# Optimization experiments

Hardware: AMD Instinct MI355X
Metric: run time of the kernel (lower is better)

## Reference

```python
import jax, jax.numpy as jnp
import numpy as np

N, E = 20000, 320000
IN_DIM, EDGE_DIM, HID = 64, 16, 64
# (in_c, heads, channels, out_c) per layer; last layer heads=1, concat=False
DIMS = [(64, 4, 64, 256), (256, 4, 64, 256), (256, 1, 64, 64)]


def _ln(x, g, b):
    m = x.mean(-1, keepdims=True)
    v = x.var(-1, keepdims=True)
    return (x - m) / jnp.sqrt(v + 1e-5) * g + b


def _gatv2(x, ei, ea, Wl, bl, Wr, br, We, att, bc, concat):
    # PyG GATv2Conv, eval mode (no dropout), add_self_loops=True, fill_value='mean'
    n = x.shape[0]
    H, C = att.shape
    ar = jnp.arange(n, dtype=ei.dtype)
    src = jnp.concatenate([ei[0], ar])
    dst = jnp.concatenate([ei[1], ar])
    ea_f = jnp.concatenate([ea, jnp.broadcast_to(ea.mean(0), (n, ea.shape[1]))], 0)
    xl = (x @ Wl + bl).reshape(n, H, C)   # source transform
    xr = (x @ Wr + br).reshape(n, H, C)   # target transform
    ee = (ea_f @ We).reshape(-1, H, C)    # edge transform (no bias in PyG)
    e = jax.nn.leaky_relu(xl[src] + xr[dst] + ee, 0.2)       # [E+N, H, C]
    score = jnp.einsum('ehc,hc->eh', e, att)                 # [E+N, H]
    mx = jax.ops.segment_max(score, dst, num_segments=n)
    a = jnp.exp(score - mx[dst])
    a = a / (jax.ops.segment_sum(a, dst, num_segments=n)[dst] + 1e-16)
    out = jax.ops.segment_sum(a[:, :, None] * xl[src], dst, num_segments=n)  # [N,H,C]
    out = out.reshape(n, H * C) if concat else out.mean(1)
    return out + bc


def _forward(x, eis, eas, Wp, bp, gp, bep, layers):
    h = jax.nn.gelu(_ln(x @ Wp + bp, gp, bep), approximate=False)
    for i in range(3):
        Wl, bl, Wr, br, We, att, bc, g, be, Wsk, bsk = layers[i]
        res = h @ Wsk + bsk
        h = _gatv2(h, eis[i], eas[i], Wl, bl, Wr, br, We, att, bc, i < 2)
        h = jax.nn.gelu(_ln(h, g, be), approximate=False) + res
    return h


def setup_inputs() -> dict:
    key = jax.random.key(0)
    ks = iter(jax.random.split(key, 64))
    rn = lambda shape, s=0.05: jax.random.normal(next(ks), shape, jnp.float32) * s
    d = {'x': jax.random.normal(next(ks), (N, IN_DIM), jnp.float32)}
    for i in range(3):
        d['ei%d' % i] = jax.random.randint(next(ks), (2, E), 0, N, jnp.int32)
        d['ea%d' % i] = jax.random.normal(next(ks), (E, EDGE_DIM), jnp.float32)
    d['Wp'] = rn((IN_DIM, HID)); d['bp'] = jnp.zeros(HID)
    d['gp'] = jnp.ones(HID); d['bep'] = jnp.zeros(HID)
    for i, (ic, H, C, oc) in enumerate(DIMS):
        hc = H * C
        d['Wl%d' % i] = rn((ic, hc)); d['bl%d' % i] = jnp.zeros(hc)
        d['Wr%d' % i] = rn((ic, hc)); d['br%d' % i] = jnp.zeros(hc)
        d['We%d' % i] = rn((EDGE_DIM, hc))
        d['att%d' % i] = rn((H, C), 0.1)
        d['bc%d' % i] = jnp.zeros(hc if i < 2 else C)
        d['g%d' % i] = jnp.ones(oc); d['be%d' % i] = jnp.zeros(oc)
        d['Wsk%d' % i] = rn((ic, oc)); d['bsk%d' % i] = jnp.zeros(oc)
    return d


def reference(x, ei0, ea0, ei1, ea1, ei2, ea2, Wp, bp, gp, bep,
              Wl0, bl0, Wr0, br0, We0, att0, bc0, g0, be0, Wsk0, bsk0,
              Wl1, bl1, Wr1, br1, We1, att1, bc1, g1, be1, Wsk1, bsk1,
              Wl2, bl2, Wr2, br2, We2, att2, bc2, g2, be2, Wsk2, bsk2):
    layers = [
        (Wl0, bl0, Wr0, br0, We0, att0, bc0, g0, be0, Wsk0, bsk0),
        (Wl1, bl1, Wr1, br1, We1, att1, bc1, g1, be1, Wsk1, bsk1),
        (Wl2, bl2, Wr2, br2, We2, att2, bc2, g2, be2, Wsk2, bsk2),
    ]
    return _forward(x, (ei0, ei1, ei2), (ea0, ea1, ea2), Wp, bp, gp, bep, layers)
```

## Files before the change

### kernel.cpp

```cpp
#include <hip/hip_runtime.h>
#include <hip/hip_bf16.h>
#include <math.h>

#define NV 20000
#define NE 320000
#define CSR_PAD 16

typedef __attribute__((ext_vector_type(8))) short bf16x8;
typedef __attribute__((ext_vector_type(4))) float f32x4;
typedef __attribute__((ext_vector_type(2))) _Float16 h2;

static __device__ __forceinline__ ushort f2b(float f) {
  __hip_bfloat16 h = __float2bfloat16(f);
  return *reinterpret_cast<ushort*>(&h);
}
static __device__ __forceinline__ float b2f(ushort u) {
  union { ushort s[2]; float f; } c;
  c.s[0] = 0; c.s[1] = u;
  return c.f;
}
static __device__ __forceinline__ ushort f2h(float f) {
  _Float16 h = (_Float16)f;
  return *reinterpret_cast<ushort*>(&h);
}
static __device__ __forceinline__ float blo(unsigned u) { return __uint_as_float(u << 16); }
static __device__ __forceinline__ float bhi(unsigned u) { return __uint_as_float(u & 0xffff0000u); }

static __device__ __forceinline__ float wave_sum64(float x) {
  x += __int_as_float(__builtin_amdgcn_update_dpp(0, __float_as_int(x), 0x111, 0xF, 0xF, true));
  x += __int_as_float(__builtin_amdgcn_update_dpp(0, __float_as_int(x), 0x112, 0xF, 0xF, true));
  x += __int_as_float(__builtin_amdgcn_update_dpp(0, __float_as_int(x), 0x114, 0xF, 0xF, true));
  x += __int_as_float(__builtin_amdgcn_update_dpp(0, __float_as_int(x), 0x118, 0xF, 0xF, true));
  x += __int_as_float(__builtin_amdgcn_update_dpp(0, __float_as_int(x), 0x142, 0xA, 0xF, true));
  x += __int_as_float(__builtin_amdgcn_update_dpp(0, __float_as_int(x), 0x143, 0xC, 0xF, true));
  return __int_as_float(__builtin_amdgcn_readlane(__float_as_int(x), 63));
}

static __device__ __forceinline__ float sum16(float x) {
  x += __int_as_float(__builtin_amdgcn_update_dpp(0, __float_as_int(x), 0x121, 0xF, 0xF, true));
  x += __int_as_float(__builtin_amdgcn_update_dpp(0, __float_as_int(x), 0x122, 0xF, 0xF, true));
  x += __int_as_float(__builtin_amdgcn_update_dpp(0, __float_as_int(x), 0x124, 0xF, 0xF, true));
  x += __int_as_float(__builtin_amdgcn_update_dpp(0, __float_as_int(x), 0x128, 0xF, 0xF, true));
  return x;
}

static __device__ __forceinline__ float dot16h(const uint4* __restrict__ E,
                                               const h2* __restrict__ Wch) {
#if __has_builtin(__builtin_amdgcn_fdot2)
  const h2* e = (const h2*)E;
  float s = 0.f;
#pragma unroll
  for (int j = 0; j < 8; ++j) s = __builtin_amdgcn_fdot2(e[j], Wch[j], s, false);
  return s;
#else
  const unsigned* u = (const unsigned*)E;
  float s = 0.f;
#pragma unroll
  for (int j = 0; j < 8; ++j) {
    union { unsigned v; h2 h; } cv; cv.v = u[j];
    s = fmaf((float)cv.h[0], (float)Wch[j][0], s);
    s = fmaf((float)cv.h[1], (float)Wch[j][1], s);
  }
  return s;
#endif
}

struct HArgs {
  const int* ei[3]; int* counts;
  const float* ea[3]; float* easum[3];
};

__global__ __launch_bounds__(256) void hist_kernel(HArgs a) {
  const int t = threadIdx.x, b = (int)blockIdx.x;
  if (b < 3750) {
    int gi = b * 256 + t;
    int l = gi / NE, i = gi - l * NE;
    atomicAdd(&a.counts[(size_t)l * (NV + 1) + a.ei[l][NE + i]], 1);
  } else {
    const int cb = b - 3750;
    const int l = cb >> 8, blk = cb & 255;
    const float4* ea4 = (const float4*)a.ea[l];
    const int cg = t & 3;
    int r = blk * 64 + (t >> 2);
    const int rstride = 256 * 64;
    float4 s = make_float4(0.f, 0.f, 0.f, 0.f);
    for (; r < NE; r += rstride) {
      float4 v = ea4[(size_t)r * 4 + cg];
      s.x += v.x; s.y += v.y; s.z += v.z; s.w += v.w;
    }
    __shared__ float4 red4[256];
    red4[t] = s;
    __syncthreads();
    if (t < 4) {
      float4 tot = make_float4(0.f, 0.f, 0.f, 0.f);
      for (int j = t; j < 256; j += 4) {
        float4 v = red4[j];
        tot.x += v.x; tot.y += v.y; tot.z += v.z; tot.w += v.w;
      }
      atomicAdd(&a.easum[l][t * 4 + 0], tot.x);
      atomicAdd(&a.easum[l][t * 4 + 1], tot.y);
      atomicAdd(&a.easum[l][t * 4 + 2], tot.z);
      atomicAdd(&a.easum[l][t * 4 + 3], tot.w);
    }
  }
}

struct CJob { const float* src; ushort* dst; int K, M; };
struct K2Args {
  const int* counts; int* offs; int* cursor;
  CJob jobs[9];
  unsigned* csr[3]; ushort* eab[3];
  const float *x, *Wp, *bp, *gp, *bep;
  ushort* h0;
};

__global__ __launch_bounds__(1024) void scan_proj_kernel(K2Args a) {
  const int b = blockIdx.x, t = threadIdx.x;
  if (b < 3) {
    const int* counts = a.counts + b * (NV + 1);
    int* offs = a.offs + b * (NV + 1);
    int* cursor = a.cursor + b * NV;
    __shared__ int ws[16];
    __shared__ int wexcl[17];
    const int lane = t & 63, wid = t >> 6;
    const int base = t * 20;
    int v[20];
    int tot = 0;
#pragma unroll
    for (int j = 0; j < 20; ++j) {
      int i = base + j;
      v[j] = (i < NV) ? counts[i] : 0;
      tot += v[j];
    }
    int x = tot;
#pragma unroll
    for (int o = 1; o < 64; o <<= 1) {
      int yy = __shfl_up(x, o, 64);
      if (lane >= o) x += yy;
    }
    if (lane == 63) ws[wid] = x;
    __syncthreads();
    if (t == 0) {
      int r = 0;
#pragma unroll
      for (int j = 0; j < 16; ++j) { wexcl[j] = r; r += ws[j]; }
      wexcl[16] = r;
    }
    __syncthreads();
    int run = wexcl[wid] + (x - tot);
#pragma unroll
    for (int j = 0; j < 20; ++j) {
      int i = base + j;
      if (i < NV) { offs[i] = run; cursor[i] = run; }
      run += v[j];
    }
    if (t == 0) offs[NV] = wexcl[16];
  } else if (b < 19) {
    if (b == 3 && t < 3 * CSR_PAD) {
      int l = t >> 4, p = t & 15;
      a.csr[l][NE + p] = 0u;
      uint4 z = make_uint4(0, 0, 0, 0);
      *(uint4*)(a.eab[l] + (size_t)(NE + p) * 16) = z;
      *(uint4*)(a.eab[l] + (size_t)(NE + p) * 16 + 8) = z;
    }
#pragma unroll
    for (int j = 0; j < 9; ++j) {
      CJob jb = a.jobs[j];
      const int total = jb.M * jb.K;
      for (int i = (b - 3) * 1024 + t; i < total; i += 16 * 1024) {
        int m = i / jb.K, k = i - m * jb.K;
        jb.dst[i] = f2b(jb.src[(size_t)k * jb.M + m]);
      }
    }
  } else {
    const int wid = t >> 6, lane = t & 63;
    const int row = (b - 19) * 16 + wid;
    float xv = a.x[(size_t)row * 64 + lane];
    float acc = a.bp[lane];
#pragma unroll
    for (int k = 0; k < 64; ++k) {
      float v = __shfl(xv, k, 64);
      acc = fmaf(v, a.Wp[k * 64 + lane], acc);
    }
    float s1 = wave_sum64(acc), s2 = wave_sum64(acc * acc);
    float mean = s1 * (1.0f / 64.0f);
    float var  = s2 * (1.0f / 64.0f) - mean * mean;
    float yv = (acc - mean) * rsqrtf(var + 1e-5f) * a.gp[lane] + a.bep[lane];
    float gel = 0.5f * yv * (1.0f + erff(yv * 0.70710678118654752f));
    a.h0[(size_t)row * 64 + lane] = f2b(gel);
  }
}

struct K3Args {
  const ushort *A, *WT;
  const float *b0, *b1, *b2;
  ushort *O0, *O1; float* O2;
  int K, M1, M2, Mtot, NT;
  const int* ei[3]; const float* ea[3];
  int* cursor;
  unsigned* csr[3]; ushort* eab[3]; int HC[3];
};

__global__ __launch_bounds__(256) void mega_kernel(K3Args a) {
  __shared__ ushort As[128][40];
  __shared__ ushort Bs[64][40];
  const int t = threadIdx.x;
  const int b = (int)blockIdx.x;
  if (b < a.NT) {
    const int wave = t >> 6, lane = t & 63;
    const int mcols = a.Mtot >> 6;
    const int col0 = (b % mcols) * 64, row0 = (b / mcols) * 128;
    const int m_ = lane & 15, q = lane >> 4;
    f32x4 acc[2][4];
#pragma unroll
    for (int i = 0; i < 2; ++i)
#pragma unroll
      for (int j = 0; j < 4; ++j) acc[i][j] = (f32x4){0.f, 0.f, 0.f, 0.f};
    const int ar = t >> 1, ac = (t & 1) * 16;
    const int br = t >> 2, bcol = (t & 3) * 8;
    const ushort* Ap = a.A + (size_t)(row0 + ar) * a.K + ac;
    const ushort* Bp = a.WT + (size_t)(col0 + br) * a.K + bcol;
    const bool a_ok = (row0 + ar) < NV;
    for (int k0 = 0; k0 < a.K; k0 += 32) {
      uint4 av0 = make_uint4(0, 0, 0, 0), av1 = make_uint4(0, 0, 0, 0);
      if (a_ok) { av0 = *(const uint4*)(Ap + k0); av1 = *(const uint4*)(Ap + k0 + 8); }
      uint4 bv = *(const uint4*)(Bp + k0);
      *(uint4*)&As[ar][ac] = av0;
      *(uint4*)&As[ar][ac + 8] = av1;
      *(uint4*)&Bs[br][bcol] = bv;
      __syncthreads();
      bf16x8 a0 = *(const bf16x8*)&As[wave * 32 + m_][q * 8];
      bf16x8 a1 = *(const bf16x8*)&As[wave * 32 + 16 + m_][q * 8];
#pragma unroll
      for (int cf = 0; cf < 4; ++cf) {
        bf16x8 bfr = *(const bf16x8*)&Bs[cf * 16 + m_][q * 8];
        acc[0][cf] = __builtin_amdgcn_mfma_f32_16x16x32_bf16(a0, bfr, acc[0][cf], 0, 0, 0);
        acc[1][cf] = __builtin_amdgcn_mfma_f32_16x16x32_bf16(a1, bfr, acc[1][cf], 0, 0, 0);
      }
      __syncthreads();
    }
    const float* bias; int base, mode, Wd;
    if (col0 < a.M1)      { bias = a.b0; base = 0;    mode = 0; Wd = a.M1; }
    else if (col0 < a.M2) { bias = a.b1; base = a.M1; mode = 1; Wd = a.M2 - a.M1; }
    else                  { bias = a.b2; base = a.M2; mode = 2; Wd = a.Mtot - a.M2; }
#pragma unroll
    for (int rf = 0; rf < 2; ++rf) {
#pragma unroll
      for (int cf = 0; cf < 4; ++cf) {
        int col = col0 + cf * 16 + m_ - base;
        float bb = bias[col];
#pragma unroll
        for (int r = 0; r < 4; ++r) {
          int row = row0 + wave * 32 + rf * 16 + q * 4 + r;
          if (row < NV) {
            float v = acc[rf][cf][r] + bb;
            if (mode == 0)      a.O0[(size_t)row * Wd + col] = f2b(v);
            else if (mode == 1) a.O1[(size_t)row * Wd + col] = f2b(v);
            else                a.O2[(size_t)row * Wd + col] = v;
          }
        }
      }
    }
  } else {
    int gi = (b - a.NT) * 256 + t;
    int l = gi / NE, i = gi - l * NE;
    int dst = a.ei[l][NE + i], src = a.ei[l][i];
    int pos = atomicAdd(&a.cursor[(size_t)l * NV + dst], 1);
    a.csr[l][pos] = (unsigned)(src * a.HC[l]);
    const float4* er = (const float4*)(a.ea[l] + (size_t)i * 16);
    float4 q0 = er[0], q1 = er[1], q2 = er[2], q3 = er[3];
    uint4 w0, w1;
    w0.x = (unsigned)f2h(q0.x) | ((unsigned)f2h(q0.y) << 16);
    w0.y = (unsigned)f2h(q0.z) | ((unsigned)f2h(q0.w) << 16);
    w0.z = (unsigned)f2h(q1.x) | ((unsigned)f2h(q1.y) << 16);
    w0.w = (unsigned)f2h(q1.z) | ((unsigned)f2h(q1.w) << 16);
    w1.x = (unsigned)f2h(q2.x) | ((unsigned)f2h(q2.y) << 16);
    w1.y = (unsigned)f2h(q2.z) | ((unsigned)f2h(q2.w) << 16);
    w1.z = (unsigned)f2h(q3.x) | ((unsigned)f2h(q3.y) << 16);
    w1.w = (unsigned)f2h(q3.z) | ((unsigned)f2h(q3.w) << 16);
    *(uint4*)(a.eab[l] + (size_t)pos * 16) = w0;
    *(uint4*)(a.eab[l] + (size_t)pos * 16 + 8) = w1;
  }
}

__global__ __launch_bounds__(256) void gemm_fused(
    const ushort* __restrict__ A, const ushort* __restrict__ WT,
    const float* __restrict__ b0, const float* __restrict__ b1,
    const float* __restrict__ b2,
    ushort* __restrict__ O0, ushort* __restrict__ O1, float* __restrict__ O2,
    int N, int K, int M1, int M2, int Mtot)
{
  __shared__ ushort As[128][40];
  __shared__ ushort Bs[64][40];
  const int t = threadIdx.x, wave = t >> 6, lane = t & 63;
  const int row0 = blockIdx.y * 128, col0 = blockIdx.x * 64;
  const int m_ = lane & 15, q = lane >> 4;
  f32x4 acc[2][4];
#pragma unroll
  for (int i = 0; i < 2; ++i)
#pragma unroll
    for (int j = 0; j < 4; ++j) acc[i][j] = (f32x4){0.f, 0.f, 0.f, 0.f};
  const int ar = t >> 1, ac = (t & 1) * 16;
  const int br = t >> 2, bcol = (t & 3) * 8;
  const ushort* Ap = A + (size_t)(row0 + ar) * K + ac;
  const ushort* Bp = WT + (size_t)(col0 + br) * K + bcol;
  const bool a_ok = (row0 + ar) < N;
  for (int k0 = 0; k0 < K; k0 += 32) {
    uint4 av0 = make_uint4(0, 0, 0, 0), av1 = make_uint4(0, 0, 0, 0);
    if (a_ok) { av0 = *(const uint4*)(Ap + k0); av1 = *(const uint4*)(Ap + k0 + 8); }
    uint4 bv = *(const uint4*)(Bp + k0);
    *(uint4*)&As[ar][ac] = av0;
    *(uint4*)&As[ar][ac + 8] = av1;
    *(uint4*)&Bs[br][bcol] = bv;
    __syncthreads();
    bf16x8 a0 = *(const bf16x8*)&As[wave * 32 + m_][q * 8];
    bf16x8 a1 = *(const bf16x8*)&As[wave * 32 + 16 + m_][q * 8];
#pragma unroll
    for (int cf = 0; cf < 4; ++cf) {
      bf16x8 bfr = *(const bf16x8*)&Bs[cf * 16 + m_][q * 8];
      acc[0][cf] = __builtin_amdgcn_mfma_f32_16x16x32_bf16(a0, bfr, acc[0][cf], 0, 0, 0);
      acc[1][cf] = __builtin_amdgcn_mfma_f32_16x16x32_bf16(a1, bfr, acc[1][cf], 0, 0, 0);
    }
    __syncthreads();
  }
  const float* bias; int base, mode, Wd;
  if (col0 < M1)      { bias = b0; base = 0;  mode = 0; Wd = M1; }
  else if (col0 < M2) { bias = b1; base = M1; mode = 1; Wd = M2 - M1; }
  else                { bias = b2; base = M2; mode = 2; Wd = Mtot - M2; }
#pragma unroll
  for (int rf = 0; rf < 2; ++rf) {
#pragma unroll
    for (int cf = 0; cf < 4; ++cf) {
      int col = col0 + cf * 16 + m_ - base;
      float bb = bias[col];
#pragma unroll
      for (int r = 0; r < 4; ++r) {
        int row = row0 + wave * 32 + rf * 16 + q * 4 + r;
        if (row < N) {
          float v = acc[rf][cf][r] + bb;
          if (mode == 0)      O0[(size_t)row * Wd + col] = f2b(v);
          else if (mode == 1) O1[(size_t)row * Wd + col] = f2b(v);
          else                O2[(size_t)row * Wd + col] = v;
        }
      }
    }
  }
}

__global__ __launch_bounds__(256) void agg4_kernel(
    const ushort* __restrict__ eab, const float* __restrict__ easum,
    const float* __restrict__ We,
    const ushort* __restrict__ xl, const ushort* __restrict__ xr,
    const float* __restrict__ att, const float* __restrict__ bc,
    const float* __restrict__ g, const float* __restrict__ be,
    const float* __restrict__ res,
    const int* __restrict__ offs, const unsigned* __restrict__ csr,
    ushort* __restrict__ houtb, int E)
{
  const int t = threadIdx.x, lane = t & 63, wave = t >> 6;
  const int n = blockIdx.x * 4 + wave;
  const int cb = 4 * lane;
  const size_t rowb = (size_t)n * 256 + cb;
  const float L2E = 1.4426950408889634f;

  float4 atv = *(const float4*)(att + cb);
  float at[4] = {atv.x * L2E, atv.y * L2E, atv.z * L2E, atv.w * L2E};

  h2 Wch[4][8];
  float esf[4] = {0.f, 0.f, 0.f, 0.f};
#pragma unroll
  for (int k = 0; k < 8; ++k) {
    float4 wr0 = *(const float4*)(We + (2 * k) * 256 + cb);
    float4 wr1 = *(const float4*)(We + (2 * k + 1) * 256 + cb);
    const float* w0 = &wr0.x;
    const float* w1 = &wr1.x;
    float e0 = easum[2 * k], e1 = easum[2 * k + 1];
#pragma unroll
    for (int j = 0; j < 4; ++j) {
      esf[j] = fmaf(e0, w0[j], esf[j]);
      esf[j] = fmaf(e1, w1[j], esf[j]);
      Wch[j][k] = (h2){(_Float16)w0[j], (_Float16)w1[j]};
    }
  }
#pragma unroll
  for (int j = 0; j < 4; ++j) esf[j] *= 1.0f / (float)E;

  uint2 qr = *(const uint2*)(xr + rowb);
  float xrv[4] = {blo(qr.x), bhi(qr.x), blo(qr.y), bhi(qr.y)};
  uint2 qn = *(const uint2*)(xl + rowb);
  float xln[4] = {blo(qn.x), bhi(qn.x), blo(qn.y), bhi(qn.y)};

  float p = 0.f;
#pragma unroll
  for (int j = 0; j < 4; ++j) {
    float v = xln[j] + xrv[j] + esf[j];
    v = v > 0.f ? v : 0.2f * v;
    p = fmaf(v, at[j], p);
  }
  float wself = exp2f(sum16(p));
  float acc[4];
#pragma unroll
  for (int j = 0; j < 4; ++j) acc[j] = wself * xln[j];
  float denom = wself;

  const int beg = __builtin_amdgcn_readfirstlane(offs[n]);
  const int end = __builtin_amdgcn_readfirstlane(offs[n + 1]);

  unsigned P[2];
  uint4 EA[2][2];
  uint2 XL[2];
#pragma unroll
  for (int k = 0; k < 2; ++k) {
    P[k] = csr[beg + k];
    const uint4* ep = (const uint4*)(eab + (size_t)(beg + k) * 16);
    EA[k][0] = ep[0]; EA[k][1] = ep[1];
  }
#pragma unroll
  for (int k = 0; k < 2; ++k)
    XL[k] = *(const uint2*)(xl + __builtin_amdgcn_readfirstlane(P[k]) + cb);

  for (int idx = beg; idx < end; idx += 2) {
    unsigned Q[2];
    uint4 EB[2][2];
    uint2 XN[2];
#pragma unroll
    for (int k = 0; k < 2; ++k) Q[k] = csr[idx + 2 + k];
#pragma unroll
    for (int k = 0; k < 2; ++k) {
      const uint4* ep = (const uint4*)(eab + (size_t)(idx + 2 + k) * 16);
      EB[k][0] = ep[0]; EB[k][1] = ep[1];
    }
#pragma unroll
    for (int k = 0; k < 2; ++k)
      XN[k] = *(const uint2*)(xl + __builtin_amdgcn_readfirstlane(Q[k]) + cb);

#pragma unroll
    for (int k = 0; k < 2; ++k) {
      float xf[4] = {blo(XL[k].x), bhi(XL[k].x), blo(XL[k].y), bhi(XL[k].y)};
      float pp = 0.f;
#pragma unroll
      for (int j = 0; j < 4; ++j) {
        float ee = dot16h(EA[k], Wch[j]);
        float v = xf[j] + xrv[j] + ee;
        v = v > 0.f ? v : 0.2f * v;
        pp = fmaf(v, at[j], pp);
      }
      float S = sum16(pp);
      float w = (idx + k < end) ? exp2f(S) : 0.f;
#pragma unroll
      for (int j = 0; j < 4; ++j) acc[j] = fmaf(w, xf[j], acc[j]);
      denom += w;
    }
#pragma unroll
    for (int k = 0; k < 2; ++k) { P[k] = Q[k]; EA[k][0] = EB[k][0]; EA[k][1] = EB[k][1]; XL[k] = XN[k]; }
  }

  const float inv = 1.0f / (denom + 1e-16f);
  float4 bcv = *(const float4*)(bc + cb);
  float out[4];
  out[0] = acc[0] * inv + bcv.x; out[1] = acc[1] * inv + bcv.y;
  out[2] = acc[2] * inv + bcv.z; out[3] = acc[3] * inv + bcv.w;

  float so1 = out[0] + out[1] + out[2] + out[3];
  float so2 = out[0] * out[0] + out[1] * out[1] + out[2] * out[2] + out[3] * out[3];
  float s1 = wave_sum64(so1), s2 = wave_sum64(so2);
  float mean = s1 * (1.0f / 256.0f);
  float var  = s2 * (1.0f / 256.0f) - mean * mean;
  float rstd = rsqrtf(var + 1e-5f);
  float4 gv = *(const float4*)(g + cb);
  float4 bev = *(const float4*)(be + cb);
  float4 rv = *(const float4*)(res + rowb);
  const float* gp = &gv.x; const float* bep = &bev.x; const float* rp = &rv.x;
  ushort ob[4];
#pragma unroll
  for (int j = 0; j < 4; ++j) {
    float y = (out[j] - mean) * rstd * gp[j] + bep[j];
    float gel = 0.5f * y * (1.0f + erff(y * 0.70710678118654752f));
    ob[j] = f2b(gel + rp[j]);
  }
  uint2 ov;
  ov.x = (unsigned)ob[0] | ((unsigned)ob[1] << 16);
  ov.y = (unsigned)ob[2] | ((unsigned)ob[3] << 16);
  *(uint2*)(houtb + rowb) = ov;
}

__global__ __launch_bounds__(256, 4) void agg1_kernel(
    const ushort* __restrict__ eab, const float* __restrict__ easum,
    const float* __restrict__ We,
    const ushort* __restrict__ xl, const ushort* __restrict__ xr,
    const float* __restrict__ att, const float* __restrict__ bc,
    const float* __restrict__ g, const float* __restrict__ be,
    const float* __restrict__ res,
    const int* __restrict__ offs, const unsigned* __restrict__ csr,
    float* __restrict__ houtf, int E)
{
  const int HC = 64;
  const int t = threadIdx.x, lane = t & 63, wave = t >> 6;
  const int n = blockIdx.x * 4 + wave;
  const int c = lane;

  const float xr_t = b2f(xr[(size_t)n * HC + c]);
  const float att_t = att[c] * 1.4426950408889634f;
  float eself = 0.f;
  h2 Wch[8];
#pragma unroll
  for (int j = 0; j < 8; ++j) {
    float w0 = We[(2 * j) * HC + c], w1 = We[(2 * j + 1) * HC + c];
    eself = fmaf(easum[2 * j], w0, eself);
    eself = fmaf(easum[2 * j + 1], w1, eself);
    Wch[j] = (h2){(_Float16)w0, (_Float16)w1};
  }
  eself *= 1.0f / (float)E;

  const float xln = b2f(xl[(size_t)n * HC + c]);
  float vs = xln + xr_t + eself;
  vs = vs > 0.f ? vs : 0.2f * vs;
  const float wself = exp2f(wave_sum64(vs * att_t));
  float acc = wself * xln, denom = wself;

  const int beg = __builtin_amdgcn_readfirstlane(offs[n]);
  const int end = __builtin_amdgcn_readfirstlane(offs[n + 1]);

  unsigned P[4];
  uint4 EA[4][2];
  float XL[4];
#pragma unroll
  for (int k = 0; k < 4; ++k) {
    P[k] = csr[beg + k];
    const uint4* ep = (const uint4*)(eab + (size_t)(beg + k) * 16);
    EA[k][0] = ep[0]; EA[k][1] = ep[1];
  }
#pragma unroll
  for (int k = 0; k < 4; ++k)
    XL[k] = b2f(xl[__builtin_amdgcn_readfirstlane(P[k]) + c]);

  for (int idx = beg; idx < end; idx += 4) {
    unsigned Q[4];
    uint4 EB[4][2];
    float XLN[4];
#pragma unroll
    for (int k = 0; k < 4; ++k) Q[k] = csr[idx + 4 + k];
#pragma unroll
    for (int k = 0; k < 4; ++k) {
      const uint4* ep = (const uint4*)(eab + (size_t)(idx + 4 + k) * 16);
      EB[k][0] = ep[0]; EB[k][1] = ep[1];
    }
#pragma unroll
    for (int k = 0; k < 4; ++k)
      XLN[k] = b2f(xl[__builtin_amdgcn_readfirstlane(Q[k]) + c]);

    float wv[4];
#pragma unroll
    for (int k = 0; k < 4; ++k) {
      float ee = dot16h(EA[k], Wch);
      float v = XL[k] + xr_t + ee;
      v = v > 0.f ? v : 0.2f * v;
      float S = wave_sum64(v * att_t);
      wv[k] = (idx + k < end) ? exp2f(S) : 0.f;
    }
#pragma unroll
    for (int k = 0; k < 4; ++k) { acc = fmaf(wv[k], XL[k], acc); denom += wv[k]; }
#pragma unroll
    for (int k = 0; k < 4; ++k) {
      P[k] = Q[k]; EA[k][0] = EB[k][0]; EA[k][1] = EB[k][1]; XL[k] = XLN[k];
    }
  }

  float out = acc / (denom + 1e-16f) + bc[c];
  float s1 = wave_sum64(out), s2 = wave_sum64(out * out);
  float mean = s1 / (float)HC;
  float var  = s2 / (float)HC - mean * mean;
  float y = (out - mean) * rsqrtf(var + 1e-5f) * g[c] + be[c];
  float gel = 0.5f * y * (1.0f + erff(y * 0.70710678118654752f));
  houtf[(size_t)n * HC + c] = gel + res[(size_t)n * HC + c];
}

extern "C" void kernel_launch(void* const* d_in, const int* in_sizes, int n_in,
                              void* d_out, int out_size, void* d_ws, size_t ws_size,
                              hipStream_t stream)
{
  auto in = [&](int i) { return (const float*)d_in[i]; };

  const int ic[3] = {64, 256, 256}, hc[3] = {256, 256, 64}, oc[3] = {256, 256, 64};
  const int CSRN = NE + CSR_PAD;

  char* w = (char*)d_ws;
  size_t off = 0;
  auto alloc = [&](size_t bytes) { void* p = w + off; off = (off + bytes + 511) & ~(size_t)511; return p; };
  ushort* B1   = (ushort*)alloc((size_t)NV * 256 * 2);
  ushort* B2   = (ushort*)alloc((size_t)NV * 256 * 2);
  float*  B3   = (float*)alloc((size_t)NV * 256 * 4);
  ushort* h0bf = (ushort*)alloc((size_t)NV * 64 * 2);
  ushort* h1bf = (ushort*)alloc((size_t)NV * 256 * 2);
  ushort* h2bf = (ushort*)alloc((size_t)NV * 256 * 2);
  ushort* Wcat[3];
  for (int i = 0; i < 3; ++i)
    Wcat[i] = (ushort*)alloc((size_t)(2 * hc[i] + oc[i]) * ic[i] * 2);
  float*    easumA  = (float*)alloc(3 * 64);
  int*      countsA = (int*)alloc((size_t)3 * (NV + 1) * 4);
  int*      offsA   = (int*)alloc((size_t)3 * (NV + 1) * 4);
  int*      cursorA = (int*)alloc((size_t)3 * NV * 4);
  unsigned* csrA    = (unsigned*)alloc((size_t)3 * CSRN * 4);
  ushort*   eabA    = (ushort*)alloc((size_t)3 * CSRN * 16 * 2);

  hipMemsetAsync(easumA, 0, 512 + (size_t)3 * (NV + 1) * 4, stream);

  HArgs ha;
  for (int i = 0; i < 3; ++i) {
    ha.ei[i] = (const int*)d_in[1 + 2 * i];
    ha.ea[i] = in(2 + 2 * i);
    ha.easum[i] = easumA + i * 16;
  }
  ha.counts = countsA;
  hist_kernel<<<3750 + 768, 256, 0, stream>>>(ha);

  K2Args k2;
  k2.counts = countsA; k2.offs = offsA; k2.cursor = cursorA;
  for (int i = 0; i < 3; ++i) {
    k2.jobs[i * 3 + 0] = {in(11 + 11 * i), Wcat[i],                             ic[i], hc[i]};
    k2.jobs[i * 3 + 1] = {in(13 + 11 * i), Wcat[i] + (size_t)hc[i] * ic[i],     ic[i], hc[i]};
    k2.jobs[i * 3 + 2] = {in(20 + 11 * i), Wcat[i] + (size_t)2 * hc[i] * ic[i], ic[i], oc[i]};
    k2.csr[i] = csrA + (size_t)i * CSRN;
    k2.eab[i] = eabA + (size_t)i * CSRN * 16;
  }
  k2.x = in(0); k2.Wp = in(7); k2.bp = in(8); k2.gp = in(9); k2.bep = in(10);
  k2.h0 = h0bf;
  scan_proj_kernel<<<19 + NV / 16, 1024, 0, stream>>>(k2);

  K3Args ga;
  ga.A = h0bf; ga.WT = Wcat[0];
  ga.b0 = in(12); ga.b1 = in(14); ga.b2 = in(21);
  ga.O0 = B1; ga.O1 = B2; ga.O2 = B3;
  ga.K = 64; ga.M1 = 256; ga.M2 = 512; ga.Mtot = 768;
  ga.NT = (768 / 64) * ((NV + 127) / 128);
  for (int i = 0; i < 3; ++i) {
    ga.ei[i] = (const int*)d_in[1 + 2 * i];
    ga.ea[i] = in(2 + 2 * i);
    ga.csr[i] = csrA + (size_t)i * CSRN;
    ga.eab[i] = eabA + (size_t)i * CSRN * 16;
    ga.HC[i] = hc[i];
  }
  ga.cursor = cursorA;
  mega_kernel<<<ga.NT + 3750, 256, 0, stream>>>(ga);

  agg4_kernel<<<NV / 4, 256, 0, stream>>>(
      eabA + 0, easumA + 0, in(15), B1, B2, in(16), in(17), in(18), in(19),
      B3, offsA, csrA, h1bf, NE);

  gemm_fused<<<dim3(768 / 64, (NV + 127) / 128), 256, 0, stream>>>(
      h1bf, Wcat[1], in(23), in(25), in(32), B1, B2, B3, NV, 256, 256, 512, 768);

  agg4_kernel<<<NV / 4, 256, 0, stream>>>(
      eabA + (size_t)CSRN * 16, easumA + 16, in(26), B1, B2, in(27), in(28),
      in(29), in(30), B3, offsA + (NV + 1), csrA + (size_t)CSRN, h2bf, NE);

  gemm_fused<<<dim3(192 / 64, (NV + 127) / 128), 256, 0, stream>>>(
      h2bf, Wcat[2], in(34), in(36), in(43), B1, B2, B3, NV, 256, 64, 128, 192);

  agg1_kernel<<<NV / 4, 256, 0, stream>>>(
      eabA + (size_t)2 * CSRN * 16, easumA + 32, in(37), B1, B2, in(38), in(39),
      in(40), in(41), B3, offsA + 2 * (NV + 1), csrA + (size_t)2 * CSRN,
      (float*)d_out, NE);
}
```

Baseline: 542.1 us.

## Split each node's edge aggregation across two waves and precompute packed edge weights

The aggregation kernels now give each destination node two waves that walk even and odd CSR edges, then merge partial sums and denominators through shared memory, doubling the grid. The fp16-packed edge weights and the self-loop mean-edge term are precomputed once in an extra block of the scan kernel, so no wave repeats that setup. The edge dot product now seeds its accumulator with xl+xr to save an add. This targets per-node latency on long serial edge loops, at the cost of a block-wide sync, shared-memory traffic, and half the waves idling through the epilogue.

```diff
diff --git a/kernel.cpp b/kernel.cpp
--- a/kernel.cpp
+++ b/kernel.cpp
@@ -25,6 +25,9 @@
 }
 static __device__ __forceinline__ float blo(unsigned u) { return __uint_as_float(u << 16); }
 static __device__ __forceinline__ float bhi(unsigned u) { return __uint_as_float(u & 0xffff0000u); }
+static __device__ __forceinline__ h2 u2h2(unsigned u) {
+  union { unsigned v; h2 h; } c; c.v = u; return c.h;
+}
 
 static __device__ __forceinline__ float wave_sum64(float x) {
   x += __int_as_float(__builtin_amdgcn_update_dpp(0, __float_as_int(x), 0x111, 0xF, 0xF, true));
@@ -44,17 +47,16 @@
   return x;
 }
 
-static __device__ __forceinline__ float dot16h(const uint4* __restrict__ E,
-                                               const h2* __restrict__ Wch) {
+static __device__ __forceinline__ float dot16h_i(const uint4* __restrict__ E,
+                                                 const h2* __restrict__ Wch,
+                                                 float s) {
 #if __has_builtin(__builtin_amdgcn_fdot2)
   const h2* e = (const h2*)E;
-  float s = 0.f;
 #pragma unroll
   for (int j = 0; j < 8; ++j) s = __builtin_amdgcn_fdot2(e[j], Wch[j], s, false);
   return s;
 #else
   const unsigned* u = (const unsigned*)E;
-  float s = 0.f;
 #pragma unroll
   for (int j = 0; j < 8; ++j) {
     union { unsigned v; h2 h; } cv; cv.v = u[j];
@@ -112,6 +114,10 @@
   unsigned* csr[3]; ushort* eab[3];
   const float *x, *Wp, *bp, *gp, *bep;
   ushort* h0;
+  const float* easum;
+  const float* We[3];
+  unsigned* wchx[3];
+  float* esfO[3];
 };
 
 __global__ __launch_bounds__(1024) void scan_proj_kernel(K2Args a) {
@@ -172,7 +178,7 @@
         jb.dst[i] = f2b(jb.src[(size_t)k * jb.M + m]);
       }
     }
-  } else {
+  } else if (b < 19 + NV / 16) {
     const int wid = t >> 6, lane = t & 63;
     const int row = (b - 19) * 16 + wid;
     float xv = a.x[(size_t)row * 64 + lane];
@@ -188,6 +194,34 @@
     float yv = (acc - mean) * rsqrtf(var + 1e-5f) * a.gp[lane] + a.bep[lane];
     float gel = 0.5f * yv * (1.0f + erff(yv * 0.70710678118654752f));
     a.h0[(size_t)row * 64 + lane] = f2b(gel);
+  } else {
+    for (int i = t; i < 4608; i += 1024) {
+      int l, e;
+      if (i < 2048)      { l = 0; e = i; }
+      else if (i < 4096) { l = 1; e = i - 2048; }
+      else               { l = 2; e = i - 4096; }
+      const int hcl = (l == 2) ? 64 : 256;
+      int k8 = e / hcl, c = e - k8 * hcl;
+      const float* We = a.We[l];
+      a.wchx[l][e] = (unsigned)f2h(We[(2 * k8) * hcl + c]) |
+                     ((unsigned)f2h(We[(2 * k8 + 1) * hcl + c]) << 16);
+    }
+    for (int i = t; i < 576; i += 1024) {
+      int l, c;
+      if (i < 256)      { l = 0; c = i; }
+      else if (i < 512) { l = 1; c = i - 256; }
+      else              { l = 2; c = i - 512; }
+      const int hcl = (l == 2) ? 64 : 256;
+      const float* We = a.We[l];
+      const float* es = a.easum + l * 16;
+      float s = 0.f;
+#pragma unroll
+      for (int k8 = 0; k8 < 8; ++k8) {
+        s = fmaf(es[2 * k8], We[(2 * k8) * hcl + c], s);
+        s = fmaf(es[2 * k8 + 1], We[(2 * k8 + 1) * hcl + c], s);
+      }
+      a.esfO[l][c] = s * (1.0f / (float)NE);
+    }
   }
 }
 
@@ -348,17 +382,19 @@
 }
 
 __global__ __launch_bounds__(256) void agg4_kernel(
-    const ushort* __restrict__ eab, const float* __restrict__ easum,
-    const float* __restrict__ We,
+    const ushort* __restrict__ eab, const unsigned* __restrict__ wchx,
+    const float* __restrict__ esf,
     const ushort* __restrict__ xl, const ushort* __restrict__ xr,
     const float* __restrict__ att, const float* __restrict__ bc,
     const float* __restrict__ g, const float* __restrict__ be,
     const float* __restrict__ res,
     const int* __restrict__ offs, const unsigned* __restrict__ csr,
-    ushort* __restrict__ houtb, int E)
+    ushort* __restrict__ houtb)
 {
-  const int t = threadIdx.x, lane = t & 63, wave = t >> 6;
-  const int n = blockIdx.x * 4 + wave;
+  __shared__ float mrg[4][64][5];
+  const int t = threadIdx.x, lane = t & 63, wid = t >> 6;
+  const int n = blockIdx.x * 2 + (wid >> 1);
+  const int par = wid & 1;
   const int cb = 4 * lane;
   const size_t rowb = (size_t)n * 256 + cb;
   const float L2E = 1.4426950408889634f;
@@ -367,43 +403,37 @@
   float at[4] = {atv.x * L2E, atv.y * L2E, atv.z * L2E, atv.w * L2E};
 
   h2 Wch[4][8];
-  float esf[4] = {0.f, 0.f, 0.f, 0.f};
-#pragma unroll
-  for (int k = 0; k < 8; ++k) {
-    float4 wr0 = *(const float4*)(We + (2 * k) * 256 + cb);
-    float4 wr1 = *(const float4*)(We + (2 * k + 1) * 256 + cb);
-    const float* w0 = &wr0.x;
-    const float* w1 = &wr1.x;
-    float e0 = easum[2 * k], e1 = easum[2 * k + 1];
-#pragma unroll
-    for (int j = 0; j < 4; ++j) {
-      esf[j] = fmaf(e0, w0[j], esf[j]);
-      esf[j] = fmaf(e1, w1[j], esf[j]);
-      Wch[j][k] = (h2){(_Float16)w0[j], (_Float16)w1[j]};
-    }
-  }
-#pragma unroll
-  for (int j = 0; j < 4; ++j) esf[j] *= 1.0f / (float)E;
+#pragma unroll
+  for (int k8 = 0; k8 < 8; ++k8) {
+    uint4 wv = *(const uint4*)(wchx + k8 * 256 + cb);
+    Wch[0][k8] = u2h2(wv.x); Wch[1][k8] = u2h2(wv.y);
+    Wch[2][k8] = u2h2(wv.z); Wch[3][k8] = u2h2(wv.w);
+  }
+  float4 esfv = *(const float4*)(esf + cb);
+  const float* esfp = &esfv.x;
 
   uint2 qr = *(const uint2*)(xr + rowb);
   float xrv[4] = {blo(qr.x), bhi(qr.x), blo(qr.y), bhi(qr.y)};
   uint2 qn = *(const uint2*)(xl + rowb);
   float xln[4] = {blo(qn.x), bhi(qn.x), blo(qn.y), bhi(qn.y)};
 
-  float p = 0.f;
-#pragma unroll
-  for (int j = 0; j < 4; ++j) {
-    float v = xln[j] + xrv[j] + esf[j];
-    v = v > 0.f ? v : 0.2f * v;
-    p = fmaf(v, at[j], p);
-  }
-  float wself = exp2f(sum16(p));
-  float acc[4];
-#pragma unroll
-  for (int j = 0; j < 4; ++j) acc[j] = wself * xln[j];
-  float denom = wself;
-
-  const int beg = __builtin_amdgcn_readfirstlane(offs[n]);
+  float acc[4] = {0.f, 0.f, 0.f, 0.f};
+  float denom = 0.f;
+  if (par == 0) {
+    float p = 0.f;
+#pragma unroll
+    for (int j = 0; j < 4; ++j) {
+      float v = xln[j] + xrv[j] + esfp[j];
+      v = v > 0.f ? v : 0.2f * v;
+      p = fmaf(v, at[j], p);
+    }
+    float wself = exp2f(sum16(p));
+#pragma unroll
+    for (int j = 0; j < 4; ++j) acc[j] = wself * xln[j];
+    denom = wself;
+  }
+
+  const int beg = __builtin_amdgcn_readfirstlane(offs[n]) + par;
   const int end = __builtin_amdgcn_readfirstlane(offs[n + 1]);
 
   unsigned P[2];
@@ -411,23 +441,23 @@
   uint2 XL[2];
 #pragma unroll
   for (int k = 0; k < 2; ++k) {
-    P[k] = csr[beg + k];
-    const uint4* ep = (const uint4*)(eab + (size_t)(beg + k) * 16);
+    P[k] = csr[beg + 2 * k];
+    const uint4* ep = (const uint4*)(eab + (size_t)(beg + 2 * k) * 16);
     EA[k][0] = ep[0]; EA[k][1] = ep[1];
   }
 #pragma unroll
   for (int k = 0; k < 2; ++k)
     XL[k] = *(const uint2*)(xl + __builtin_amdgcn_readfirstlane(P[k]) + cb);
 
-  for (int idx = beg; idx < end; idx += 2) {
+  for (int idx = beg; idx < end; idx += 4) {
     unsigned Q[2];
     uint4 EB[2][2];
     uint2 XN[2];
 #pragma unroll
-    for (int k = 0; k < 2; ++k) Q[k] = csr[idx + 2 + k];
+    for (int k = 0; k < 2; ++k) Q[k] = csr[idx + 4 + 2 * k];
 #pragma unroll
     for (int k = 0; k < 2; ++k) {
-      const uint4* ep = (const uint4*)(eab + (size_t)(idx + 2 + k) * 16);
+      const uint4* ep = (const uint4*)(eab + (size_t)(idx + 4 + 2 * k) * 16);
       EB[k][0] = ep[0]; EB[k][1] = ep[1];
     }
 #pragma unroll
@@ -440,20 +470,31 @@
       float pp = 0.f;
 #pragma unroll
       for (int j = 0; j < 4; ++j) {
-        float ee = dot16h(EA[k], Wch[j]);
-        float v = xf[j] + xrv[j] + ee;
+        float v = dot16h_i(EA[k], Wch[j], xf[j] + xrv[j]);
         v = v > 0.f ? v : 0.2f * v;
         pp = fmaf(v, at[j], pp);
       }
       float S = sum16(pp);
-      float w = (idx + k < end) ? exp2f(S) : 0.f;
+      float w = (idx + 2 * k < end) ? exp2f(S) : 0.f;
 #pragma unroll
       for (int j = 0; j < 4; ++j) acc[j] = fmaf(w, xf[j], acc[j]);
       denom += w;
     }
 #pragma unroll
-    for (int k = 0; k < 2; ++k) { P[k] = Q[k]; EA[k][0] = EB[k][0]; EA[k][1] = EB[k][1]; XL[k] = XN[k]; }
-  }
+    for (int k = 0; k < 2; ++k) {
+      P[k] = Q[k]; EA[k][0] = EB[k][0]; EA[k][1] = EB[k][1]; XL[k] = XN[k];
+    }
+  }
+
+#pragma unroll
+  for (int j = 0; j < 4; ++j) mrg[wid][lane][j] = acc[j];
+  mrg[wid][lane][4] = denom;
+  __syncthreads();
+  const int pw = wid ^ 1;
+#pragma unroll
+  for (int j = 0; j < 4; ++j) acc[j] += mrg[pw][lane][j];
+  denom += mrg[pw][lane][4];
+  if (par) return;
 
   const float inv = 1.0f / (denom + 1e-16f);
   float4 bcv = *(const float4*)(bc + cb);
@@ -485,86 +526,88 @@
 }
 
 __global__ __launch_bounds__(256, 4) void agg1_kernel(
-    const ushort* __restrict__ eab, const float* __restrict__ easum,
-    const float* __restrict__ We,
+    const ushort* __restrict__ eab, const unsigned* __restrict__ wchx,
+    const float* __restrict__ esf,
     const ushort* __restrict__ xl, const ushort* __restrict__ xr,
     const float* __restrict__ att, const float* __restrict__ bc,
     const float* __restrict__ g, const float* __restrict__ be,
     const float* __restrict__ res,
     const int* __restrict__ offs, const unsigned* __restrict__ csr,
-    float* __restrict__ houtf, int E)
+    float* __restrict__ houtf)
 {
   const int HC = 64;
-  const int t = threadIdx.x, lane = t & 63, wave = t >> 6;
-  const int n = blockIdx.x * 4 + wave;
+  __shared__ float mrg[4][64][2];
+  const int t = threadIdx.x, lane = t & 63, wid = t >> 6;
+  const int n = blockIdx.x * 2 + (wid >> 1);
+  const int par = wid & 1;
   const int c = lane;
 
   const float xr_t = b2f(xr[(size_t)n * HC + c]);
   const float att_t = att[c] * 1.4426950408889634f;
-  float eself = 0.f;
   h2 Wch[8];
 #pragma unroll
-  for (int j = 0; j < 8; ++j) {
-    float w0 = We[(2 * j) * HC + c], w1 = We[(2 * j + 1) * HC + c];
-    eself = fmaf(easum[2 * j], w0, eself);
-    eself = fmaf(easum[2 * j + 1], w1, eself);
-    Wch[j] = (h2){(_Float16)w0, (_Float16)w1};
-  }
-  eself *= 1.0f / (float)E;
-
+  for (int k8 = 0; k8 < 8; ++k8) Wch[k8] = u2h2(wchx[k8 * 64 + c]);
+  const float eself = esf[c];
   const float xln = b2f(xl[(size_t)n * HC + c]);
-  float vs = xln + xr_t + eself;
-  vs = vs > 0.f ? vs : 0.2f * vs;
-  const float wself = exp2f(wave_sum64(vs * att_t));
-  float acc = wself * xln, denom = wself;
-
-  const int beg = __builtin_amdgcn_readfirstlane(offs[n]);
+
+  float acc = 0.f, denom = 0.f;
+  if (par == 0) {
+    float vs = xln + xr_t + eself;
+    vs = vs > 0.f ? vs : 0.2f * vs;
+    float wself = exp2f(wave_sum64(vs * att_t));
+    acc = wself * xln; denom = wself;
+  }
+
+  const int beg = __builtin_amdgcn_readfirstlane(offs[n]) + par;
   const int end = __builtin_amdgcn_readfirstlane(offs[n + 1]);
 
-  unsigned P[4];
-  uint4 EA[4][2];
-  float XL[4];
-#pragma unroll
-  for (int k = 0; k < 4; ++k) {
-    P[k] = csr[beg + k];
-    const uint4* ep = (const uint4*)(eab + (size_t)(beg + k) * 16);
+  unsigned P[2];
+  uint4 EA[2][2];
+  float XL[2];
+#pragma unroll
+  for (int k = 0; k < 2; ++k) {
+    P[k] = csr[beg + 2 * k];
+    const uint4* ep = (const uint4*)(eab + (size_t)(beg + 2 * k) * 16);
     EA[k][0] = ep[0]; EA[k][1] = ep[1];
   }
 #pragma unroll
-  for (int k = 0; k < 4; ++k)
+  for (int k = 0; k < 2; ++k)
     XL[k] = b2f(xl[__builtin_amdgcn_readfirstlane(P[k]) + c]);
 
   for (int idx = beg; idx < end; idx += 4) {
-    unsigned Q[4];
-    uint4 EB[4][2];
-    float XLN[4];
-#pragma unroll
-    for (int k = 0; k < 4; ++k) Q[k] = csr[idx + 4 + k];
-#pragma unroll
-    for (int k = 0; k < 4; ++k) {
-      const uint4* ep = (const uint4*)(eab + (size_t)(idx + 4 + k) * 16);
+    unsigned Q[2];
+    uint4 EB[2][2];
+    float XLN[2];
+#pragma unroll
+    for (int k = 0; k < 2; ++k) Q[k] = csr[idx + 4 + 2 * k];
+#pragma unroll
+    for (int k = 0; k < 2; ++k) {
+      const uint4* ep = (const uint4*)(eab + (size_t)(idx + 4 + 2 * k) * 16);
       EB[k][0] = ep[0]; EB[k][1] = ep[1];
     }
 #pragma unroll
-    for (int k = 0; k < 4; ++k)
+    for (int k = 0; k < 2; ++k)
       XLN[k] = b2f(xl[__builtin_amdgcn_readfirstlane(Q[k]) + c]);
 
-    float wv[4];
-#pragma unroll
-    for (int k = 0; k < 4; ++k) {
-      float ee = dot16h(EA[k], Wch);
-      float v = XL[k] + xr_t + ee;
+#pragma unroll
+    for (int k = 0; k < 2; ++k) {
+      float v = dot16h_i(EA[k], Wch, XL[k] + xr_t);
       v = v > 0.f ? v : 0.2f * v;
       float S = wave_sum64(v * att_t);
-      wv[k] = (idx + k < end) ? exp2f(S) : 0.f;
-    }
-#pragma unroll
-    for (int k = 0; k < 4; ++k) { acc = fmaf(wv[k], XL[k], acc); denom += wv[k]; }
-#pragma unroll
-    for (int k = 0; k < 4; ++k) {
+      float w = (idx + 2 * k < end) ? exp2f(S) : 0.f;
+      acc = fmaf(w, XL[k], acc); denom += w;
+    }
+#pragma unroll
+    for (int k = 0; k < 2; ++k) {
       P[k] = Q[k]; EA[k][0] = EB[k][0]; EA[k][1] = EB[k][1]; XL[k] = XLN[k];
     }
   }
+
+  mrg[wid][lane][0] = acc; mrg[wid][lane][1] = denom;
+  __syncthreads();
+  acc += mrg[wid ^ 1][lane][0];
+  denom += mrg[wid ^ 1][lane][1];
+  if (par) return;
 
   float out = acc / (denom + 1e-16f) + bc[c];
   float s1 = wave_sum64(out), s2 = wave_sum64(out * out);
@@ -602,6 +645,8 @@
   int*      cursorA = (int*)alloc((size_t)3 * NV * 4);
   unsigned* csrA    = (unsigned*)alloc((size_t)3 * CSRN * 4);
   ushort*   eabA    = (ushort*)alloc((size_t)3 * CSRN * 16 * 2);
+  unsigned* wchxA   = (unsigned*)alloc((size_t)4608 * 4);
+  float*    esfA    = (float*)alloc((size_t)576 * 4);
 
   hipMemsetAsync(easumA, 0, 512 + (size_t)3 * (NV + 1) * 4, stream);
 
@@ -622,10 +667,14 @@
     k2.jobs[i * 3 + 2] = {in(20 + 11 * i), Wcat[i] + (size_t)2 * hc[i] * ic[i], ic[i], oc[i]};
     k2.csr[i] = csrA + (size_t)i * CSRN;
     k2.eab[i] = eabA + (size_t)i * CSRN * 16;
+    k2.We[i] = in(15 + 11 * i);
   }
   k2.x = in(0); k2.Wp = in(7); k2.bp = in(8); k2.gp = in(9); k2.bep = in(10);
   k2.h0 = h0bf;
-  scan_proj_kernel<<<19 + NV / 16, 1024, 0, stream>>>(k2);
+  k2.easum = easumA;
+  k2.wchx[0] = wchxA; k2.wchx[1] = wchxA + 2048; k2.wchx[2] = wchxA + 4096;
+  k2.esfO[0] = esfA; k2.esfO[1] = esfA + 256; k2.esfO[2] = esfA + 512;
+  scan_proj_kernel<<<19 + NV / 16 + 1, 1024, 0, stream>>>(k2);
 
   K3Args ga;
   ga.A = h0bf; ga.WT = Wcat[0];
@@ -643,22 +692,22 @@
   ga.cursor = cursorA;
   mega_kernel<<<ga.NT + 3750, 256, 0, stream>>>(ga);
 
-  agg4_kernel<<<NV / 4, 256, 0, stream>>>(
-      eabA + 0, easumA + 0, in(15), B1, B2, in(16), in(17), in(18), in(19),
-      B3, offsA, csrA, h1bf, NE);
+  agg4_kernel<<<NV / 2, 256, 0, stream>>>(
+      eabA + 0, wchxA, esfA, B1, B2, in(16), in(17), in(18), in(19),
+      B3, offsA, csrA, h1bf);
 
   gemm_fused<<<dim3(768 / 64, (NV + 127) / 128), 256, 0, stream>>>(
       h1bf, Wcat[1], in(23), in(25), in(32), B1, B2, B3, NV, 256, 256, 512, 768);
 
-  agg4_kernel<<<NV / 4, 256, 0, stream>>>(
-      eabA + (size_t)CSRN * 16, easumA + 16, in(26), B1, B2, in(27), in(28),
-      in(29), in(30), B3, offsA + (NV + 1), csrA + (size_t)CSRN, h2bf, NE);
+  agg4_kernel<<<NV / 2, 256, 0, stream>>>(
+      eabA + (size_t)CSRN * 16, wchxA + 2048, esfA + 256, B1, B2, in(27), in(28),
+      in(29), in(30), B3, offsA + (NV + 1), csrA + (size_t)CSRN, h2bf);
 
   gemm_fused<<<dim3(192 / 64, (NV + 127) / 128), 256, 0, stream>>>(
       h2bf, Wcat[2], in(34), in(36), in(43), B1, B2, B3, NV, 256, 64, 128, 192);
 
-  agg1_kernel<<<NV / 4, 256, 0, stream>>>(
-      eabA + (size_t)2 * CSRN * 16, easumA + 32, in(37), B1, B2, in(38), in(39),
+  agg1_kernel<<<NV / 2, 256, 0, stream>>>(
+      eabA + (size_t)2 * CSRN * 16, wchxA + 4096, esfA + 512, B1, B2, in(38), in(39),
       in(40), in(41), B3, offsA + 2 * (NV + 1), csrA + (size_t)2 * CSRN,
-      (float*)d_out, NE);
-}
+      (float*)d_out);
+}
```

Result: no change. 548.0 us (+1.1%).
